# Kernel optimization log

Hardware: AMD Instinct MI355X
Metric: run time of the kernel (lower is better)

The kernel has to match this reference:

```python
import jax, jax.numpy as jnp
import numpy as np

N, C_IN, C_OUT, HID, H = 4096, 512, 512, 128, 4
HEAD_OUT = C_OUT // H  # 128
MID = 4 * C_OUT        # 2048
R = 1.0                # spatial radius r
L = 48                 # sequence window l
NEG = -1e9


def layer_norm(x, g, b, eps=1e-5):
    m = jnp.mean(x, axis=-1, keepdims=True)
    v = jnp.mean(jnp.square(x - m), axis=-1, keepdims=True)
    return (x - m) * jax.lax.rsqrt(v + eps) * g + b


def setup_inputs() -> dict:
    key = jax.random.key(0)
    ks = jax.random.split(key, 16)
    s = lambda fan: 1.0 / np.sqrt(fan)
    return {
        "x":   jax.random.normal(ks[0], (N, C_IN), jnp.float32),
        "pos": jax.random.normal(ks[1], (N, 3), jnp.float32),
        "ori": jax.random.normal(ks[2], (N, 3), jnp.float32),
        "seq": jnp.arange(N, dtype=jnp.int64) if jax.config.jax_enable_x64 else jnp.arange(N, dtype=jnp.int32),
        "batch": jnp.sort(jax.random.randint(ks[3], (N,), 0, 8)),
        "ln1_g": jnp.ones((C_IN,), jnp.float32),
        "ln1_b": jnp.zeros((C_IN,), jnp.float32),
        "ln2_g": jnp.ones((C_OUT,), jnp.float32),
        "ln2_b": jnp.zeros((C_OUT,), jnp.float32),
        "Wq": jax.random.normal(ks[4], (H, C_IN, HID), jnp.float32) * s(C_IN),
        "Wk": jax.random.normal(ks[5], (H, C_IN, HID), jnp.float32) * s(C_IN),
        "Wv": jax.random.normal(ks[6], (H, C_IN, HID), jnp.float32) * s(C_IN),
        "Wo": jax.random.normal(ks[7], (H, HID, HEAD_OUT), jnp.float32) * s(HID),
        "lnm_g": jnp.ones((MID,), jnp.float32),
        "lnm_b": jnp.zeros((MID,), jnp.float32),
        "W1": jax.random.normal(ks[8], (C_OUT, MID), jnp.float32) * s(C_OUT),
        "W2": jax.random.normal(ks[9], (MID, C_OUT), jnp.float32) * s(MID),
    }


def _block(x, pos, ori, seq, batch, ln1_g, ln1_b, ln2_g, ln2_b,
           Wq, Wk, Wv, Wo, lnm_g, lnm_b, W1, W2):
    identity = x
    xn = layer_norm(x, ln1_g, ln1_b)

    # geometry/sequence neighborhood mask: same graph, ||dp||<=r, |ds|<=l
    d2 = jnp.sum(jnp.square(pos[:, None, :] - pos[None, :, :]), axis=-1)  # [N,N]
    ds = jnp.abs(seq[:, None] - seq[None, :])
    mask = (batch[:, None] == batch[None, :]) & (d2 <= R * R) & (ds <= L)

    # all heads at once (original loops over heads; math identical)
    q = jnp.einsum('nc,hcd->hnd', xn, Wq)
    k = jnp.einsum('nc,hcd->hnd', xn, Wk)
    v = jnp.einsum('nc,hcd->hnd', xn, Wv)
    gbias = ori @ ori.T  # geometric orientation bias [N,N]
    scores = jnp.einsum('hnd,hmd->hnm', q, k) / np.sqrt(HID) + gbias[None]
    scores = jnp.where(mask[None], scores, NEG)
    attn = jax.nn.softmax(scores, axis=-1)
    o = jnp.einsum('hnm,hmd->hnd', attn, v)
    o = jnp.einsum('hnd,hde->hne', o, Wo)               # [H,N,HEAD_OUT]
    o = jnp.transpose(o, (1, 0, 2)).reshape(N, C_OUT)   # concat heads

    x = o + identity
    identity = x
    h = layer_norm(x, ln2_g, ln2_b) @ W1
    h = jax.nn.relu(layer_norm(h, lnm_g, lnm_b))
    return h @ W2 + identity


def reference(x, pos, ori, seq, batch, ln1_g, ln1_b, ln2_g, ln2_b,
              Wq, Wk, Wv, Wo, lnm_g, lnm_b, W1, W2):
    return _block(x, pos, ori, seq, batch, ln1_g, ln1_b, ln2_g, ln2_b,
                  Wq, Wk, Wv, Wo, lnm_g, lnm_b, W1, W2)
```

## Files before the change

### kernel.cpp

```cpp
#include <hip/hip_runtime.h>

typedef unsigned short u16;
typedef unsigned int u32;
typedef float f32x4 __attribute__((ext_vector_type(4)));
typedef __bf16 bf16x8 __attribute__((ext_vector_type(8)));

#define N_TOK 4096
#define QKV_LD 1536
#define NH 4
#define HID 128
#define C_OUT 512

__device__ __forceinline__ float b2f(u16 u) { return __uint_as_float(((u32)u) << 16); }
__device__ __forceinline__ u16 f2b(float f) {
  u32 u = __float_as_uint(f);
  u32 r = (u + 0x7fffu + ((u >> 16) & 1u)) >> 16;
  return (u16)r;
}

__device__ __forceinline__ void gload16(const u16* g, u16* l) {
  __builtin_amdgcn_global_load_lds(
      (const __attribute__((address_space(1))) void*)g,
      (__attribute__((address_space(3))) void*)l, 16, 0, 0);
}

__device__ __forceinline__ void tr32(const float* __restrict__ s,
                                     u16* __restrict__ d, int R, int C,
                                     int r0, int c0, u16 (*tile)[33]) {
  const int tx = threadIdx.x & 31, ty = threadIdx.x >> 5;
#pragma unroll
  for (int i = 0; i < 32; i += 8)
    tile[ty + i][tx] = f2b(s[(size_t)(r0 + ty + i) * C + c0 + tx]);
  __syncthreads();
#pragma unroll
  for (int i = 0; i < 32; i += 8)
    d[(size_t)(c0 + ty + i) * R + r0 + tx] = tile[tx][ty + i];
}

__device__ __forceinline__ void tr32_512(const float* __restrict__ s,
                                         u16* __restrict__ d, int R, int C,
                                         int r0, int c0, u16 (*tile)[33]) {
  const int tx = threadIdx.x & 31, ty = threadIdx.x >> 5;
#pragma unroll
  for (int i = 0; i < 32; i += 16)
    tile[ty + i][tx] = f2b(s[(size_t)(r0 + ty + i) * C + c0 + tx]);
  __syncthreads();
#pragma unroll
  for (int i = 0; i < 32; i += 16)
    d[(size_t)(c0 + ty + i) * R + r0 + tx] = tile[tx][ty + i];
}

__device__ __forceinline__ void ln512_body(
    const float* __restrict__ x, const float* __restrict__ g,
    const float* __restrict__ b, u16* __restrict__ y, int row) {
  const int lane = threadIdx.x & 63;
  const float* xr = x + (size_t)row * 512;
  const int c = lane * 8;
  float4 a0 = *(const float4*)(xr + c);
  float4 a1 = *(const float4*)(xr + c + 4);
  float v[8] = {a0.x, a0.y, a0.z, a0.w, a1.x, a1.y, a1.z, a1.w};
  float s1 = 0.f, s2 = 0.f;
#pragma unroll
  for (int i = 0; i < 8; i++) { s1 += v[i]; s2 += v[i] * v[i]; }
#pragma unroll
  for (int o = 32; o; o >>= 1) { s1 += __shfl_xor(s1, o); s2 += __shfl_xor(s2, o); }
  float mean = s1 * (1.f / 512.f);
  float var = s2 * (1.f / 512.f) - mean * mean;
  float rs = rsqrtf(fmaxf(var, 0.f) + 1e-5f);
  float4 g0 = *(const float4*)(g + c), g1 = *(const float4*)(g + c + 4);
  float4 b0 = *(const float4*)(b + c), b1 = *(const float4*)(b + c + 4);
  float gg[8] = {g0.x, g0.y, g0.z, g0.w, g1.x, g1.y, g1.z, g1.w};
  float bb[8] = {b0.x, b0.y, b0.z, b0.w, b1.x, b1.y, b1.z, b1.w};
  u16 t[8];
#pragma unroll
  for (int i = 0; i < 8; i++) t[i] = f2b((v[i] - mean) * rs * gg[i] + bb[i]);
  *(uint4*)(y + (size_t)row * 512 + c) = *(const uint4*)t;
}

__global__ __launch_bounds__(256) void prep(
    const float* __restrict__ x, const float* __restrict__ ln1g,
    const float* __restrict__ ln1b, u16* __restrict__ xn,
    const float* __restrict__ Wq, const float* __restrict__ Wk,
    const float* __restrict__ Wv, const float* __restrict__ Wo,
    const float* __restrict__ W1,
    u16* __restrict__ Btqkv, u16* __restrict__ Wot, u16* __restrict__ W1t)
{
  __shared__ u16 tile[32][33];
  const int bid = blockIdx.x;
  if (bid < 1024) {
    ln512_body(x, ln1g, ln1b, xn, bid * 4 + (threadIdx.x >> 6));
    return;
  }
  const int idx = bid - 1024;
  const float* s; u16* d; int R, C, r0, c0;
  if (idx < 1024) {
    s = W1; d = W1t; R = 512; C = 2048;
    r0 = (idx >> 6) * 32; c0 = (idx & 63) * 32;
  } else if (idx < 1792) {
    int i = idx - 1024;
    int z = i >> 6, rem = i & 63;
    int which = z >> 2, b = z & 3;
    const float* base = (which == 0) ? Wq : (which == 1) ? Wk : Wv;
    s = base + (size_t)b * 512 * 128;
    d = Btqkv + (size_t)which * 4 * 512 * 128 + (size_t)b * 512 * 128;
    R = 512; C = 128;
    r0 = (rem >> 2) * 32; c0 = (rem & 3) * 32;
  } else {
    int i = idx - 1792;
    int b = i >> 4, rem = i & 15;
    s = Wo + (size_t)b * 128 * 128;
    d = Wot + (size_t)b * 128 * 128;
    R = 128; C = 128;
    r0 = (rem >> 2) * 32; c0 = (rem & 3) * 32;
  }
  tr32(s, d, R, C, r0, c0, tile);
}

__global__ __launch_bounds__(256) void ln512_f32(
    const float* __restrict__ x, const float* __restrict__ g,
    const float* __restrict__ b, u16* __restrict__ y)
{
  ln512_body(x, g, b, y, blockIdx.x * 4 + (threadIdx.x >> 6));
}

__global__ __launch_bounds__(256) void ln2048_bf16_relu(
    const u16* __restrict__ x, const float* __restrict__ g,
    const float* __restrict__ b, u16* __restrict__ y)
{
  const int row = blockIdx.x, tid = threadIdx.x;
  const int c = tid * 8;
  const u16* xr = x + (size_t)row * 2048;
  uint4 u = *(const uint4*)(xr + c);
  u16 e[8]; *(uint4*)e = u;
  float v[8];
#pragma unroll
  for (int i = 0; i < 8; i++) v[i] = b2f(e[i]);
  float s1 = 0.f, s2 = 0.f;
#pragma unroll
  for (int i = 0; i < 8; i++) { s1 += v[i]; s2 += v[i] * v[i]; }
#pragma unroll
  for (int o = 32; o; o >>= 1) { s1 += __shfl_xor(s1, o); s2 += __shfl_xor(s2, o); }
  __shared__ float red[2][4];
  int lane = tid & 63, w = tid >> 6;
  if (lane == 0) { red[0][w] = s1; red[1][w] = s2; }
  __syncthreads();
  s1 = red[0][0] + red[0][1] + red[0][2] + red[0][3];
  s2 = red[1][0] + red[1][1] + red[1][2] + red[1][3];
  float mean = s1 * (1.f / 2048.f);
  float var = s2 * (1.f / 2048.f) - mean * mean;
  float rs = rsqrtf(fmaxf(var, 0.f) + 1e-5f);
  float4 g0 = *(const float4*)(g + c), g1 = *(const float4*)(g + c + 4);
  float4 b0 = *(const float4*)(b + c), b1 = *(const float4*)(b + c + 4);
  float gg[8] = {g0.x, g0.y, g0.z, g0.w, g1.x, g1.y, g1.z, g1.w};
  float bb[8] = {b0.x, b0.y, b0.z, b0.w, b1.x, b1.y, b1.z, b1.w};
  u16 t[8];
#pragma unroll
  for (int i = 0; i < 8; i++)
    t[i] = f2b(fmaxf((v[i] - mean) * rs * gg[i] + bb[i], 0.f));
  *(uint4*)(y + (size_t)row * 2048 + c) = *(const uint4*)t;
}

__global__ __launch_bounds__(512, 4) void gemm128(
    const u16* __restrict__ A, int lda,
    const u16* __restrict__ Bt,
    void* __restrict__ C, int ldc, int outf32,
    const float* __restrict__ res,
    int Kslice, int Ktot, int atomic)
{
  __shared__ u16 As[2][128 * 64];
  __shared__ u16 Bs[2][128 * 64];
  const int id = blockIdx.x + gridDim.x * blockIdx.y;
  const int xr = id & 7, xj = id >> 3;
  const int bm = xr * 4 + (xj & 3);
  const int bn = xj >> 2;
  const int m0 = bm * 128, n0 = bn * 128;
  const int kbase = blockIdx.z * Kslice;
  const int tid = threadIdx.x;
  const int lane = tid & 63, w = tid >> 6;
  const int wm = (w & 1) * 64;
  const int wn = (w >> 1) * 32;
  const int l16 = lane & 15, quad = lane >> 4;

  const int sr = tid >> 3;
  const int sch = (tid & 7) ^ (sr & 7);
  const u16* PA = A + (size_t)(m0 + sr) * lda + kbase + sch * 8;
  const u16* PB = Bt + (size_t)(n0 + sr) * Ktot + kbase + sch * 8;
  const size_t askip = (size_t)64 * lda;
  const size_t bskip = (size_t)64 * Ktot;

  f32x4 acc[4][2];
#pragma unroll
  for (int i = 0; i < 4; i++)
#pragma unroll
    for (int j = 0; j < 2; j++) acc[i][j] = (f32x4){0.f, 0.f, 0.f, 0.f};

  {
    gload16(PA, &As[0][w * 512]);
    gload16(PA + askip, &As[0][4096 + w * 512]);
    gload16(PB, &Bs[0][w * 512]);
    gload16(PB + bskip, &Bs[0][4096 + w * 512]);
  }
  __syncthreads();

  int buf = 0;
  for (int kk = 0; kk < Kslice; kk += 64) {
    if (kk + 64 < Kslice) {
      PA += 64; PB += 64;
      gload16(PA, &As[buf ^ 1][w * 512]);
      gload16(PA + askip, &As[buf ^ 1][4096 + w * 512]);
      gload16(PB, &Bs[buf ^ 1][w * 512]);
      gload16(PB + bskip, &Bs[buf ^ 1][4096 + w * 512]);
    }
#pragma unroll
    for (int kc = 0; kc < 2; kc++) {
      bf16x8 af[4], bfr[2];
#pragma unroll
      for (int mt = 0; mt < 4; mt++) {
        int row = wm + mt * 16 + l16;
        af[mt] = *(const bf16x8*)&As[buf][row * 64 + (((kc * 4 + quad) ^ (row & 7)) * 8)];
      }
#pragma unroll
      for (int nt = 0; nt < 2; nt++) {
        int row = wn + nt * 16 + l16;
        bfr[nt] = *(const bf16x8*)&Bs[buf][row * 64 + (((kc * 4 + quad) ^ (row & 7)) * 8)];
      }
#pragma unroll
      for (int mt = 0; mt < 4; mt++)
#pragma unroll
        for (int nt = 0; nt < 2; nt++)
          acc[mt][nt] = __builtin_amdgcn_mfma_f32_16x16x32_bf16(
              af[mt], bfr[nt], acc[mt][nt], 0, 0, 0);
    }
    __syncthreads();
    buf ^= 1;
  }

#pragma unroll
  for (int mt = 0; mt < 4; mt++)
#pragma unroll
    for (int nt = 0; nt < 2; nt++)
#pragma unroll
      for (int r = 0; r < 4; r++) {
        int gr = m0 + wm + mt * 16 + quad * 4 + r;
        int gc = n0 + wn + nt * 16 + l16;
        size_t off = (size_t)gr * ldc + gc;
        float v = acc[mt][nt][r];
        if (atomic) {
          atomicAdd((float*)C + off, v);
        } else {
          if (res) v += res[off];
          if (outf32) ((float*)C)[off] = v;
          else        ((u16*)C)[off] = f2b(v);
        }
      }
}

#define TQ 32
#define BAND 128
#define QROW 136
#define PROW 132
__global__ __launch_bounds__(512) void attn_mfma(
    const u16* __restrict__ qkv, const float* __restrict__ pos,
    const float* __restrict__ ori, const int* __restrict__ batch,
    const u16* __restrict__ wot, const float* __restrict__ xres,
    float* __restrict__ out,
    const float* __restrict__ W2, u16* __restrict__ W2t)
{
  __shared__ u16 kv[128 * 128];
  __shared__ u16 qp[TQ * QROW];
  __shared__ float ps[TQ * PROW];
  __shared__ float bpx[BAND], bpy[BAND], bpz[BAND];
  __shared__ float box_[BAND], boy_[BAND], boz_[BAND];
  __shared__ int bb[BAND];

  if (blockIdx.x >= 128) {
    int idx = (blockIdx.x - 128) + blockIdx.y * 256;
    int r0 = (idx >> 4) * 32, c0 = (idx & 15) * 32;
    tr32_512(W2, W2t, 2048, 512, r0, c0, (u16(*)[33])kv);
    return;
  }

  const int h = blockIdx.y;
  const int bxs = (blockIdx.x & 7) * 16 + (blockIdx.x >> 3);
  const int i0 = bxs * TQ;
  const int j0 = i0 - 48;
  const int tid = threadIdx.x;
  const int lane = tid & 63, w = tid >> 6;
  const int l16 = lane & 15, quad = lane >> 4;

  bf16x8 wof[4];
  {
    const u16* wsrc = wot + (size_t)h * HID * HID + (w * 16 + l16) * HID;
#pragma unroll
    for (int kc = 0; kc < 4; kc++)
      wof[kc] = *(const bf16x8*)&wsrc[kc * 32 + quad * 8];
  }

  if (tid < BAND) {
    int t = tid, j = j0 + t;
    if (j >= 0 && j < N_TOK) {
      bpx[t] = pos[j * 3 + 0]; bpy[t] = pos[j * 3 + 1]; bpz[t] = pos[j * 3 + 2];
      box_[t] = ori[j * 3 + 0]; boy_[t] = ori[j * 3 + 1]; boz_[t] = ori[j * 3 + 2];
      bb[t] = batch[j];
    } else {
      bpx[t] = bpy[t] = bpz[t] = 0.f;
      box_[t] = boy_[t] = boz_[t] = 0.f;
      bb[t] = -12345;
    }
  }
  {
    const u16* kbase = qkv + 512 + h * HID;
#pragma unroll
    for (int call = 0; call < 4; call++) {
      int row = call * 32 + w * 4 + (lane >> 4);
      int c = (lane & 15) ^ (row & 15);
      const u16* g = kbase + (size_t)(j0 + row) * QKV_LD + c * 8;
      gload16(g, &kv[call * 4096 + w * 512]);
    }
  }
  {
    int q = tid >> 4, c8 = (tid & 15) * 8;
    *(int4*)&qp[q * QROW + c8] =
        *(const int4*)&qkv[(size_t)(i0 + q) * QKV_LD + h * HID + c8];
  }
  __syncthreads();

  {
    const int t = w * 16 + l16;
    bf16x8 bf[4];
#pragma unroll
    for (int kc = 0; kc < 4; kc++)
      bf[kc] = *(const bf16x8*)&kv[t * 128 + (((kc * 4 + quad) ^ (t & 15)) * 8)];
#pragma unroll
    for (int qt = 0; qt < 2; qt++) {
      bf16x8 af[4];
#pragma unroll
      for (int kc = 0; kc < 4; kc++)
        af[kc] = *(const bf16x8*)&qp[(qt * 16 + l16) * QROW + kc * 32 + quad * 8];
      f32x4 acc = (f32x4){0.f, 0.f, 0.f, 0.f};
#pragma unroll
      for (int kc = 0; kc < 4; kc++)
        acc = __builtin_amdgcn_mfma_f32_16x16x32_bf16(af[kc], bf[kc], acc, 0, 0, 0);
#pragma unroll
      for (int r = 0; r < 4; r++) {
        int q = qt * 16 + quad * 4 + r, iq = q + 48;
        int dseq = iq - t;
        bool ok = (bb[t] == bb[iq]) && (dseq <= 48) && (dseq >= -48);
        {
#pragma clang fp contract(off)
          float dx = bpx[iq] - bpx[t], dy = bpy[iq] - bpy[t], dz = bpz[iq] - bpz[t];
          float d2 = dx * dx + dy * dy + dz * dz;
          ok = ok && (d2 <= 1.0f);
        }
        float s = -1e9f;
        if (ok) {
          float gb = box_[iq] * box_[t] + boy_[iq] * boy_[t] + boz_[iq] * boz_[t];
          s = acc[r] * 0.08838834764831845f + gb;
        }
        ps[q * PROW + t] = s;
      }
    }
  }
  __syncthreads();

  for (int idx = tid; idx < BAND * 32; idx += 512) {
    int t = idx >> 5, d4 = (idx & 31) * 4;
    int j = j0 + t;
    uint2 val; val.x = 0; val.y = 0;
    if (j >= 0 && j < N_TOK)
      val = *(const uint2*)&qkv[(size_t)j * QKV_LD + 1024 + h * HID + d4];
    u16 e[4] = {(u16)val.x, (u16)(val.x >> 16), (u16)val.y, (u16)(val.y >> 16)};
    int ct = t >> 3, cw = t & 7;
#pragma unroll
    for (int jj = 0; jj < 4; jj++) {
      int dd = (jj + tid) & 3;
      int d = d4 + dd;
      kv[d * 128 + ((ct ^ (d & 15)) * 8) + cw] = e[dd];
    }
  }
  {
    int row = tid >> 4, sub = tid & 15;
    float vals[8];
    float m = -1e30f;
#pragma unroll
    for (int i = 0; i < 8; i++) {
      vals[i] = ps[row * PROW + sub + i * 16];
      m = fmaxf(m, vals[i]);
    }
#pragma unroll
    for (int o = 8; o; o >>= 1) m = fmaxf(m, __shfl_xor(m, o));
    float s = 0.f;
#pragma unroll
    for (int i = 0; i < 8; i++) { vals[i] = __expf(vals[i] - m); s += vals[i]; }
#pragma unroll
    for (int o = 8; o; o >>= 1) s += __shfl_xor(s, o);
    float inv = 1.f / s;
#pragma unroll
    for (int i = 0; i < 8; i++)
      qp[row * QROW + sub + i * 16] = f2b(vals[i] * inv);
  }
  __syncthreads();

  u16 obuf[2][4];
  {
    const int d = w * 16 + l16;
    bf16x8 bf[4];
#pragma unroll
    for (int kc = 0; kc < 4; kc++)
      bf[kc] = *(const bf16x8*)&kv[d * 128 + (((kc * 4 + quad) ^ (d & 15)) * 8)];
#pragma unroll
    for (int qt = 0; qt < 2; qt++) {
      bf16x8 paf[4];
#pragma unroll
      for (int kc = 0; kc < 4; kc++)
        paf[kc] = *(const bf16x8*)&qp[(qt * 16 + l16) * QROW + kc * 32 + quad * 8];
      f32x4 acc = (f32x4){0.f, 0.f, 0.f, 0.f};
#pragma unroll
      for (int kc = 0; kc < 4; kc++)
        acc = __builtin_amdgcn_mfma_f32_16x16x32_bf16(paf[kc], bf[kc], acc, 0, 0, 0);
#pragma unroll
      for (int r = 0; r < 4; r++) obuf[qt][r] = f2b(acc[r]);
    }
  }
  __syncthreads();

#pragma unroll
  for (int qt = 0; qt < 2; qt++) {
#pragma unroll
    for (int r = 0; r < 4; r++)
      qp[(qt * 16 + quad * 4 + r) * QROW + w * 16 + l16] = obuf[qt][r];
  }
  __syncthreads();

  {
#pragma unroll
    for (int qt = 0; qt < 2; qt++) {
      bf16x8 oaf[4];
#pragma unroll
      for (int kc = 0; kc < 4; kc++)
        oaf[kc] = *(const bf16x8*)&qp[(qt * 16 + l16) * QROW + kc * 32 + quad * 8];
      f32x4 acc = (f32x4){0.f, 0.f, 0.f, 0.f};
#pragma unroll
      for (int kc = 0; kc < 4; kc++)
        acc = __builtin_amdgcn_mfma_f32_16x16x32_bf16(oaf[kc], wof[kc], acc, 0, 0, 0);
#pragma unroll
      for (int r = 0; r < 4; r++) {
        int q = qt * 16 + quad * 4 + r;
        size_t off = (size_t)(i0 + q) * C_OUT + h * HID + w * 16 + l16;
        out[off] = acc[r] + xres[off];
      }
    }
  }
}

#define MB (1048576)
extern "C" void kernel_launch(void* const* d_in, const int* in_sizes, int n_in,
                              void* d_out, int out_size, void* d_ws, size_t ws_size,
                              hipStream_t stream) {
  const float* x    = (const float*)d_in[0];
  const float* pos  = (const float*)d_in[1];
  const float* ori  = (const float*)d_in[2];
  const int*   batch = (const int*)d_in[4];
  const float* ln1g = (const float*)d_in[5];
  const float* ln1b = (const float*)d_in[6];
  const float* ln2g = (const float*)d_in[7];
  const float* ln2b = (const float*)d_in[8];
  const float* Wq = (const float*)d_in[9];
  const float* Wk = (const float*)d_in[10];
  const float* Wv = (const float*)d_in[11];
  const float* Wo = (const float*)d_in[12];
  const float* lnmg = (const float*)d_in[13];
  const float* lnmb = (const float*)d_in[14];
  const float* W1 = (const float*)d_in[15];
  const float* W2 = (const float*)d_in[16];
  float* out = (float*)d_out;

  char* ws = (char*)d_ws;
  u16* xn    = (u16*)(ws + 0);
  u16* x1n   = (u16*)(ws + 0);
  u16* qkv   = (u16*)(ws + 4 * MB);
  u16* h     = (u16*)(ws + 4 * MB);
  u16* Wot   = (u16*)(ws + 16 * MB);
  u16* Btqkv = (u16*)(ws + 20 * MB);
  u16* W2t   = (u16*)(ws + 20 * MB);
  u16* W1t   = (u16*)(ws + 22 * MB);

  prep<<<dim3(2880), 256, 0, stream>>>(x, ln1g, ln1b, xn,
                                       Wq, Wk, Wv, Wo, W1, Btqkv, Wot, W1t);
  gemm128<<<dim3(12, 32, 1), 512, 0, stream>>>(xn, 512, Btqkv, qkv, QKV_LD, 0,
                                               nullptr, 512, 512, 0);
  attn_mfma<<<dim3(384, NH), 512, 0, stream>>>(qkv, pos, ori, batch, Wot, x, out,
                                               W2, W2t);
  ln512_f32<<<dim3(1024), 256, 0, stream>>>(out, ln2g, ln2b, x1n);
  gemm128<<<dim3(16, 32, 1), 512, 0, stream>>>(x1n, 512, W1t, h, 2048, 0,
                                               nullptr, 512, 512, 0);
  ln2048_bf16_relu<<<dim3(4096), 256, 0, stream>>>(h, lnmg, lnmb, h);
  gemm128<<<dim3(4, 32, 2), 512, 0, stream>>>(h, 2048, W2t, out, 512, 1,
                                              nullptr, 1024, 2048, 1);
}
```

Before: 180.3 us.

## Fold LayerNorm2 into FFN1 GEMM epilogue and drop separate LN kernel

Removes the standalone ln512 kernel. The attention epilogue now also writes x*gamma as bf16, and a new FFN1 GEMM applies the normalization algebraically in its epilogue. Each block computes per-row mean and rstd from the fp32 residual, and per-column W1·gamma and W1·beta sums. The FFN2 split-K count is also raised from 2 to 4 splits. This saves one launch and one pass over the activations, but adds redundant row-statistics and column-sum work in every GEMM block, and the one-pass variance formula is less precise.

New measurement: 232.7 us. +29.0%, slower.

```diff
diff --git a/kernel.cpp b/kernel.cpp
--- a/kernel.cpp
+++ b/kernel.cpp
@@ -116,13 +116,6 @@
   tr32(s, d, R, C, r0, c0, tile);
 }
 
-__global__ __launch_bounds__(256) void ln512_f32(
-    const float* __restrict__ x, const float* __restrict__ g,
-    const float* __restrict__ b, u16* __restrict__ y)
-{
-  ln512_body(x, g, b, y, blockIdx.x * 4 + (threadIdx.x >> 6));
-}
-
 __global__ __launch_bounds__(256) void ln2048_bf16_relu(
     const u16* __restrict__ x, const float* __restrict__ g,
     const float* __restrict__ b, u16* __restrict__ y)
@@ -255,6 +248,141 @@
       }
 }
 
+__global__ __launch_bounds__(512, 4) void gemm_ffn1(
+    const u16* __restrict__ A,
+    const u16* __restrict__ Bt,
+    const float* __restrict__ outf,
+    const float* __restrict__ g2, const float* __restrict__ b2,
+    u16* __restrict__ H)
+{
+  __shared__ u16 As[2][128 * 64];
+  __shared__ u16 Bs[2][128 * 64];
+  __shared__ float meanL[128], rsL[128], uL[128], vL[128];
+  const int id = blockIdx.x + gridDim.x * blockIdx.y;
+  const int xr = id & 7, xj = id >> 3;
+  const int bm = xr * 4 + (xj & 3);
+  const int bn = xj >> 2;
+  const int m0 = bm * 128, n0 = bn * 128;
+  const int tid = threadIdx.x;
+  const int lane = tid & 63, w = tid >> 6;
+  const int wm = (w & 1) * 64;
+  const int wn = (w >> 1) * 32;
+  const int l16 = lane & 15, quad = lane >> 4;
+
+  const int sr = tid >> 3;
+  const int sch = (tid & 7) ^ (sr & 7);
+  const u16* PA = A + (size_t)(m0 + sr) * 512 + sch * 8;
+  const u16* PB = Bt + (size_t)(n0 + sr) * 512 + sch * 8;
+  const size_t askip = (size_t)64 * 512;
+
+  {
+    gload16(PA, &As[0][w * 512]);
+    gload16(PA + askip, &As[0][4096 + w * 512]);
+    gload16(PB, &Bs[0][w * 512]);
+    gload16(PB + askip, &Bs[0][4096 + w * 512]);
+  }
+
+  {
+    int r = tid >> 2, q = tid & 3;
+    const float4* p = (const float4*)(outf + (size_t)(m0 + r) * 512 + q * 128);
+    float s1 = 0.f, s2 = 0.f;
+#pragma unroll
+    for (int i = 0; i < 32; i++) {
+      float4 v4 = p[i];
+      s1 += v4.x + v4.y + v4.z + v4.w;
+      s2 += v4.x * v4.x + v4.y * v4.y + v4.z * v4.z + v4.w * v4.w;
+    }
+    s1 += __shfl_xor(s1, 1); s2 += __shfl_xor(s2, 1);
+    s1 += __shfl_xor(s1, 2); s2 += __shfl_xor(s2, 2);
+    if (q == 0) {
+      float mean = s1 * (1.f / 512.f);
+      float var = s2 * (1.f / 512.f) - mean * mean;
+      meanL[r] = mean;
+      rsL[r] = rsqrtf(fmaxf(var, 0.f) + 1e-5f);
+    }
+  }
+  {
+    int n = tid >> 2, q = tid & 3;
+    const u16* wp = Bt + (size_t)(n0 + n) * 512 + q * 128;
+    const float* gp = g2 + q * 128;
+    const float* bp = b2 + q * 128;
+    float up = 0.f, vp = 0.f;
+#pragma unroll
+    for (int i = 0; i < 16; i++) {
+      uint4 uu = *(const uint4*)(wp + i * 8);
+      u16 e[8]; *(uint4*)e = uu;
+      float4 ga = *(const float4*)(gp + i * 8);
+      float4 gb = *(const float4*)(gp + i * 8 + 4);
+      float4 ba = *(const float4*)(bp + i * 8);
+      float4 bb = *(const float4*)(bp + i * 8 + 4);
+      float wv[8];
+#pragma unroll
+      for (int j = 0; j < 8; j++) wv[j] = b2f(e[j]);
+      up += wv[0] * ga.x + wv[1] * ga.y + wv[2] * ga.z + wv[3] * ga.w
+          + wv[4] * gb.x + wv[5] * gb.y + wv[6] * gb.z + wv[7] * gb.w;
+      vp += wv[0] * ba.x + wv[1] * ba.y + wv[2] * ba.z + wv[3] * ba.w
+          + wv[4] * bb.x + wv[5] * bb.y + wv[6] * bb.z + wv[7] * bb.w;
+    }
+    up += __shfl_xor(up, 1); vp += __shfl_xor(vp, 1);
+    up += __shfl_xor(up, 2); vp += __shfl_xor(vp, 2);
+    if (q == 0) { uL[n] = up; vL[n] = vp; }
+  }
+
+  f32x4 acc[4][2];
+#pragma unroll
+  for (int i = 0; i < 4; i++)
+#pragma unroll
+    for (int j = 0; j < 2; j++) acc[i][j] = (f32x4){0.f, 0.f, 0.f, 0.f};
+
+  __syncthreads();
+
+  int buf = 0;
+  for (int kk = 0; kk < 512; kk += 64) {
+    if (kk + 64 < 512) {
+      PA += 64; PB += 64;
+      gload16(PA, &As[buf ^ 1][w * 512]);
+      gload16(PA + askip, &As[buf ^ 1][4096 + w * 512]);
+      gload16(PB, &Bs[buf ^ 1][w * 512]);
+      gload16(PB + askip, &Bs[buf ^ 1][4096 + w * 512]);
+    }
+#pragma unroll
+    for (int kc = 0; kc < 2; kc++) {
+      bf16x8 af[4], bfr[2];
+#pragma unroll
+      for (int mt = 0; mt < 4; mt++) {
+        int row = wm + mt * 16 + l16;
+        af[mt] = *(const bf16x8*)&As[buf][row * 64 + (((kc * 4 + quad) ^ (row & 7)) * 8)];
+      }
+#pragma unroll
+      for (int nt = 0; nt < 2; nt++) {
+        int row = wn + nt * 16 + l16;
+        bfr[nt] = *(const bf16x8*)&Bs[buf][row * 64 + (((kc * 4 + quad) ^ (row & 7)) * 8)];
+      }
+#pragma unroll
+      for (int mt = 0; mt < 4; mt++)
+#pragma unroll
+        for (int nt = 0; nt < 2; nt++)
+          acc[mt][nt] = __builtin_amdgcn_mfma_f32_16x16x32_bf16(
+              af[mt], bfr[nt], acc[mt][nt], 0, 0, 0);
+    }
+    __syncthreads();
+    buf ^= 1;
+  }
+
+#pragma unroll
+  for (int mt = 0; mt < 4; mt++)
+#pragma unroll
+    for (int nt = 0; nt < 2; nt++)
+#pragma unroll
+      for (int r = 0; r < 4; r++) {
+        int lr = wm + mt * 16 + quad * 4 + r;
+        int lc = wn + nt * 16 + l16;
+        float y = rsL[lr] * acc[mt][nt][r]
+                - rsL[lr] * meanL[lr] * uL[lc] + vL[lc];
+        H[(size_t)(m0 + lr) * 2048 + n0 + lc] = f2b(y);
+      }
+}
+
 #define TQ 32
 #define BAND 128
 #define QROW 136
@@ -263,7 +391,8 @@
     const u16* __restrict__ qkv, const float* __restrict__ pos,
     const float* __restrict__ ori, const int* __restrict__ batch,
     const u16* __restrict__ wot, const float* __restrict__ xres,
-    float* __restrict__ out,
+    float* __restrict__ out, u16* __restrict__ xg,
+    const float* __restrict__ ln2g,
     const float* __restrict__ W2, u16* __restrict__ W2t)
 {
   __shared__ u16 kv[128 * 128];
@@ -295,6 +424,7 @@
     for (int kc = 0; kc < 4; kc++)
       wof[kc] = *(const bf16x8*)&wsrc[kc * 32 + quad * 8];
   }
+  const float gq = ln2g[h * HID + w * 16 + l16];
 
   if (tid < BAND) {
     int t = tid, j = j0 + t;
@@ -447,7 +577,9 @@
       for (int r = 0; r < 4; r++) {
         int q = qt * 16 + quad * 4 + r;
         size_t off = (size_t)(i0 + q) * C_OUT + h * HID + w * 16 + l16;
-        out[off] = acc[r] + xres[off];
+        float v = acc[r] + xres[off];
+        out[off] = v;
+        xg[off] = f2b(v * gq);
       }
     }
   }
@@ -477,7 +609,7 @@
 
   char* ws = (char*)d_ws;
   u16* xn    = (u16*)(ws + 0);
-  u16* x1n   = (u16*)(ws + 0);
+  u16* xg    = (u16*)(ws + 0);
   u16* qkv   = (u16*)(ws + 4 * MB);
   u16* h     = (u16*)(ws + 4 * MB);
   u16* Wot   = (u16*)(ws + 16 * MB);
@@ -489,12 +621,10 @@
                                        Wq, Wk, Wv, Wo, W1, Btqkv, Wot, W1t);
   gemm128<<<dim3(12, 32, 1), 512, 0, stream>>>(xn, 512, Btqkv, qkv, QKV_LD, 0,
                                                nullptr, 512, 512, 0);
-  attn_mfma<<<dim3(384, NH), 512, 0, stream>>>(qkv, pos, ori, batch, Wot, x, out,
-                                               W2, W2t);
-  ln512_f32<<<dim3(1024), 256, 0, stream>>>(out, ln2g, ln2b, x1n);
-  gemm128<<<dim3(16, 32, 1), 512, 0, stream>>>(x1n, 512, W1t, h, 2048, 0,
-                                               nullptr, 512, 512, 0);
+  attn_mfma<<<dim3(384, NH), 512, 0, stream>>>(qkv, pos, ori, batch, Wot, x,
+                                               out, xg, ln2g, W2, W2t);
+  gemm_ffn1<<<dim3(16, 32), 512, 0, stream>>>(xg, W1t, out, ln2g, ln2b, h);
   ln2048_bf16_relu<<<dim3(4096), 256, 0, stream>>>(h, lnmg, lnmb, h);
-  gemm128<<<dim3(4, 32, 2), 512, 0, stream>>>(h, 2048, W2t, out, 512, 1,
-                                              nullptr, 1024, 2048, 1);
-}
+  gemm128<<<dim3(4, 32, 4), 512, 0, stream>>>(h, 2048, W2t, out, 512, 1,
+                                              nullptr, 512, 2048, 1);
+}
```
